# Kernel optimization log

Measured on AMD Instinct MI355X. Metric: run time of the kernel, lower is better.

## Reference

```python
import jax, jax.numpy as jnp
import numpy as np

N = 20000
E = 640000
F_IN = 128
HID = 64
HEADS = 4
OUT = 10
NUM_GRAPHS = 128
NEG_SLOPE = 0.2
BN_EPS = 1e-5


def setup_inputs() -> dict:
    key = jax.random.key(0)
    ks = jax.random.split(key, 24)
    x = jax.random.normal(ks[0], (N, F_IN), dtype=jnp.float32)
    edge_index = jax.random.randint(ks[1], (2, E), 0, N, dtype=jnp.int32)
    batch = jnp.sort(jax.random.randint(ks[2], (N,), 0, NUM_GRAPHS, dtype=jnp.int32))
    s = 0.05
    HC = HEADS * HID  # 256
    inp = {
        'x': x, 'edge_index': edge_index, 'batch': batch,
        # GATConv 1: in=128 -> heads*64, concat
        'W1': jax.random.normal(ks[3], (F_IN, HC)) * s,
        'as1': jax.random.normal(ks[4], (HEADS, HID)) * s,
        'ad1': jax.random.normal(ks[5], (HEADS, HID)) * s,
        'b1': jnp.zeros((HC,), jnp.float32),
        'g1': jnp.ones((HC,), jnp.float32),
        'be1': jnp.zeros((HC,), jnp.float32),
        # GATConv 2: in=256 -> heads*64, concat
        'W2': jax.random.normal(ks[6], (HC, HC)) * s,
        'as2': jax.random.normal(ks[7], (HEADS, HID)) * s,
        'ad2': jax.random.normal(ks[8], (HEADS, HID)) * s,
        'b2': jnp.zeros((HC,), jnp.float32),
        'g2': jnp.ones((HC,), jnp.float32),
        'be2': jnp.zeros((HC,), jnp.float32),
        # GATConv 3: in=256 -> 64, concat=False (mean over heads)
        'W3': jax.random.normal(ks[9], (HC, HC)) * s,
        'as3': jax.random.normal(ks[10], (HEADS, HID)) * s,
        'ad3': jax.random.normal(ks[11], (HEADS, HID)) * s,
        'b3': jnp.zeros((HID,), jnp.float32),
        # final Linear 64 -> 10
        'Wlin': jax.random.normal(ks[12], (HID, OUT)) * s,
        'blin': jnp.zeros((OUT,), jnp.float32),
    }
    return inp


def _gat_conv(x, src, dst, W, a_src, a_dst, b, concat):
    # PyG GATConv: h = x @ W -> [N,H,C]; alpha_e = leaky_relu(as[src]+ad[dst]);
    # softmax over edges grouped by destination; scatter-add alpha*h[src].
    h = (x @ W).reshape(N, HEADS, HID)
    a_s = jnp.einsum('nhc,hc->nh', h, a_src)  # [N,H]
    a_d = jnp.einsum('nhc,hc->nh', h, a_dst)
    e = jax.nn.leaky_relu(a_s[src] + a_d[dst], NEG_SLOPE)  # [E,H]
    m = jax.ops.segment_max(e, dst, num_segments=N)  # per-dst max, stable softmax
    e = jnp.exp(e - m[dst])
    denom = jax.ops.segment_sum(e, dst, num_segments=N)
    alpha = e / (denom[dst] + 1e-16)  # [E,H]
    out = jax.ops.segment_sum(h[src] * alpha[:, :, None], dst, num_segments=N)  # [N,H,C]
    if concat:
        out = out.reshape(N, HEADS * HID)
    else:
        out = out.mean(axis=1)
    return out + b


def _bn(x, g, b):
    # BatchNorm1d (training-mode batch statistics)
    mu = x.mean(0)
    var = x.var(0)
    return (x - mu) * jax.lax.rsqrt(var + BN_EPS) * g + b


def reference(x, edge_index, batch, W1, as1, ad1, b1, g1, be1,
              W2, as2, ad2, b2, g2, be2, W3, as3, ad3, b3, Wlin, blin):
    # add self-loops (PyG GATConv default add_self_loops=True)
    loops = jnp.arange(N, dtype=edge_index.dtype)
    src = jnp.concatenate([edge_index[0], loops])
    dst = jnp.concatenate([edge_index[1], loops])

    xs = []
    h = _gat_conv(x, src, dst, W1, as1, ad1, b1, concat=True)
    h = _bn(h, g1, be1)
    xs.append(h)
    h = jax.nn.elu(h)  # dropout is identity in eval mode

    h = _gat_conv(h, src, dst, W2, as2, ad2, b2, concat=True)
    h = _bn(h, g2, be2)
    xs.append(h)
    h = jax.nn.elu(h)

    h = _gat_conv(h, src, dst, W3, as3, ad3, b3, concat=False)
    xs.append(h)

    # global_mean_pool over graphs
    sums = jax.ops.segment_sum(h, batch, num_segments=NUM_GRAPHS)
    cnt = jax.ops.segment_sum(jnp.ones((N,), h.dtype), batch, num_segments=NUM_GRAPHS)
    pooled = sums / jnp.maximum(cnt, 1.0)[:, None]
    xs.append(pooled)

    out = pooled @ Wlin + blin
    return (out, *xs)
```

## Files before the change

### kernel.cpp

```cpp
#include <hip/hip_runtime.h>
#include <hip/hip_bf16.h>
#include <math.h>

#define N_NODES 20000
#define N_EDGES 640000
#define F_IN 128
#define HID 64
#define HEADS 4
#define HC 256
#define OUT_DIM 10
#define NUM_GRAPHS 128
#define NEG_SLOPE 0.2f
#define BN_EPS 1e-5f

typedef short bf16s;
using bf16x8 = __attribute__((ext_vector_type(8))) short;
using bf16x4 = __attribute__((ext_vector_type(4))) short;
using f32x4 = __attribute__((ext_vector_type(4))) float;

__device__ __forceinline__ float bs2f(short s) {
    unsigned int u = ((unsigned int)(unsigned short)s) << 16;
    return __builtin_bit_cast(float, u);
}
__device__ __forceinline__ short f2bs(float f) {
    unsigned int u = __builtin_bit_cast(unsigned int, f);
    unsigned int r = u + 0x7FFFu + ((u >> 16) & 1u);
    return (short)(r >> 16);
}


__global__ void fill_i32(int* p, int n, int val) {
    int tid = blockIdx.x * blockDim.x + threadIdx.x;
    if (tid < n) p[tid] = val;
}

__global__ void fill_f32(float* p, int n, float val) {
    int tid = blockIdx.x * blockDim.x + threadIdx.x;
    if (tid < n) p[tid] = val;
}

__global__ void conv_bf16(const float* __restrict__ in, bf16s* __restrict__ out, int n4) {
    int tid = blockIdx.x * blockDim.x + threadIdx.x;
    if (tid >= n4) return;
    float4 v = reinterpret_cast<const float4*>(in)[tid];
    bf16x4 o;
    o[0] = f2bs(v.x); o[1] = f2bs(v.y); o[2] = f2bs(v.z); o[3] = f2bs(v.w);
    reinterpret_cast<bf16x4*>(out)[tid] = o;
}

__global__ void prep_weights(const float* __restrict__ W1, const float* __restrict__ W2,
                             const float* __restrict__ W3,
                             bf16s* __restrict__ Wt1, bf16s* __restrict__ Wt2,
                             bf16s* __restrict__ Wt3) {
    int tid = blockIdx.x * blockDim.x + threadIdx.x;
    if (tid < HC * F_IN) {
        int c = tid >> 7, k = tid & (F_IN - 1);
        Wt1[tid] = f2bs(W1[(size_t)k * HC + c]);
    } else if (tid < HC * F_IN + HC * HC) {
        int t = tid - HC * F_IN;
        int c = t >> 8, k = t & (HC - 1);
        Wt2[t] = f2bs(W2[(size_t)k * HC + c]);
    } else if (tid < HC * F_IN + 2 * HC * HC) {
        int t = tid - HC * F_IN - HC * HC;
        int c = t >> 8, k = t & (HC - 1);
        Wt3[t] = f2bs(W3[(size_t)k * HC + c]);
    }
}


__global__ void count_deg(const int* __restrict__ ei_dst, int* deg, int E) {
    int tid = blockIdx.x * blockDim.x + threadIdx.x;
    if (tid < E) atomicAdd(&deg[ei_dst[tid]], 1);
}

__global__ void scan_deg(const int* __restrict__ deg, int* __restrict__ rowptr,
                         int* __restrict__ cursor, int n) {
    __shared__ int wsum[16];
    __shared__ int carry_s;
    int tid = threadIdx.x;
    int wid = tid >> 6, lane = tid & 63;
    if (tid == 0) { carry_s = 0; rowptr[0] = 0; }
    __syncthreads();
    for (int base = 0; base < n; base += 1024) {
        int i = base + tid;
        int v = (i < n) ? deg[i] : 0;
        int x = v;
        #pragma unroll
        for (int off = 1; off < 64; off <<= 1) {
            int t = __shfl_up(x, off);
            if (lane >= off) x += t;
        }
        if (lane == 63) wsum[wid] = x;
        __syncthreads();
        if (tid == 0) {
            int acc = carry_s;
            #pragma unroll
            for (int w = 0; w < 16; w++) { int t = wsum[w]; wsum[w] = acc; acc += t; }
            carry_s = acc;
        }
        __syncthreads();
        int inc = x + wsum[wid];
        if (i < n) { rowptr[i + 1] = inc; cursor[i] = inc - v; }
        __syncthreads();
    }
}

__global__ void fill_csr(const int* __restrict__ ei, int* cursor, int* esrc, int E, int n) {
    int tid = blockIdx.x * blockDim.x + threadIdx.x;
    if (tid < E) {
        int src = ei[tid];
        int dst = ei[E + tid];
        int pos = atomicAdd(&cursor[dst], 1);
        esrc[pos] = src;
    } else if (tid < E + n) {
        int node = tid - E;
        int pos = atomicAdd(&cursor[node], 1);
        esrc[pos] = node;
    }
}


__global__ __launch_bounds__(256) void gemm_bf16(
        const bf16s* __restrict__ A, const bf16s* __restrict__ Wt,
        bf16s* __restrict__ Hout,
        const float* __restrict__ a_src, const float* __restrict__ a_dst,
        float* __restrict__ asb, float* __restrict__ adb,
        int M, int K) {
    __shared__ bf16s As[128][72];
    __shared__ bf16s Bs[64][72];
    int tid = threadIdx.x;
    int wave = tid >> 6, lane = tid & 63;
    int row0 = blockIdx.x * 128;
    int head = blockIdx.y;
    int col0 = head * 64;
    int lr = lane & 15, lk = lane >> 4;

    f32x4 acc[2][4];
    #pragma unroll
    for (int i = 0; i < 2; i++)
        #pragma unroll
        for (int j = 0; j < 4; j++)
            acc[i][j] = (f32x4){0.f, 0.f, 0.f, 0.f};

    for (int k0 = 0; k0 < K; k0 += 64) {
        #pragma unroll
        for (int i = 0; i < 4; i++) {
            int idx = tid + i * 256;
            int r = idx >> 3, ch = idx & 7;
            int gr = row0 + r;
            bf16x8 v = {};
            if (gr < M) v = *reinterpret_cast<const bf16x8*>(A + (size_t)gr * K + k0 + ch * 8);
            *reinterpret_cast<bf16x8*>(&As[r][ch * 8]) = v;
        }
        #pragma unroll
        for (int i = 0; i < 2; i++) {
            int idx = tid + i * 256;
            int r = idx >> 3, ch = idx & 7;
            bf16x8 v = *reinterpret_cast<const bf16x8*>(Wt + (size_t)(col0 + r) * K + k0 + ch * 8);
            *reinterpret_cast<bf16x8*>(&Bs[r][ch * 8]) = v;
        }
        __syncthreads();
        #pragma unroll
        for (int ks = 0; ks < 2; ks++) {
            bf16x8 bfr[4];
            #pragma unroll
            for (int j = 0; j < 4; j++)
                bfr[j] = *reinterpret_cast<const bf16x8*>(&Bs[j * 16 + lr][ks * 32 + lk * 8]);
            #pragma unroll
            for (int i = 0; i < 2; i++) {
                bf16x8 afr = *reinterpret_cast<const bf16x8*>(&As[wave * 32 + i * 16 + lr][ks * 32 + lk * 8]);
                #pragma unroll
                for (int j = 0; j < 4; j++)
                    acc[i][j] = __builtin_amdgcn_mfma_f32_16x16x32_bf16(afr, bfr[j], acc[i][j], 0, 0, 0);
            }
        }
        __syncthreads();
    }

    #pragma unroll
    for (int i = 0; i < 2; i++) {
        #pragma unroll
        for (int q = 0; q < 4; q++) {
            int r = row0 + wave * 32 + i * 16 + lk * 4 + q;
            if (r < M) {
                #pragma unroll
                for (int j = 0; j < 4; j++) {
                    int c = col0 + j * 16 + lr;
                    Hout[(size_t)r * HC + c] = f2bs(acc[i][j][q]);
                }
            }
        }
    }

    float asv0 = a_src[col0 + 0 * 16 + lr], asv1 = a_src[col0 + 1 * 16 + lr];
    float asv2 = a_src[col0 + 2 * 16 + lr], asv3 = a_src[col0 + 3 * 16 + lr];
    float adv0 = a_dst[col0 + 0 * 16 + lr], adv1 = a_dst[col0 + 1 * 16 + lr];
    float adv2 = a_dst[col0 + 2 * 16 + lr], adv3 = a_dst[col0 + 3 * 16 + lr];
    #pragma unroll
    for (int i = 0; i < 2; i++) {
        #pragma unroll
        for (int q = 0; q < 4; q++) {
            float ps = acc[i][0][q] * asv0 + acc[i][1][q] * asv1 + acc[i][2][q] * asv2 + acc[i][3][q] * asv3;
            float pd = acc[i][0][q] * adv0 + acc[i][1][q] * adv1 + acc[i][2][q] * adv2 + acc[i][3][q] * adv3;
            #pragma unroll
            for (int off = 1; off < 16; off <<= 1) {
                ps += __shfl_xor(ps, off);
                pd += __shfl_xor(pd, off);
            }
            int r = row0 + wave * 32 + i * 16 + lk * 4 + q;
            if (lr == 0 && r < M) {
                asb[r * HEADS + head] = ps;
                adb[r * HEADS + head] = pd;
            }
        }
    }
}


__device__ __forceinline__ float lrelu(float x) { return x > 0.f ? x : NEG_SLOPE * x; }

template<int MODE>
__global__ __launch_bounds__(256) void gat_aggregate(
        const bf16s* __restrict__ hfeat,
        const float* __restrict__ asb, const float* __restrict__ adb,
        const int* __restrict__ rowptr, const int* __restrict__ esrc,
        const float* __restrict__ bias,
        float* __restrict__ out) {
    __shared__ float4 exps[4][128];
    __shared__ int    srcs[4][128];
    int wid = threadIdx.x >> 6, lane = threadIdx.x & 63;
    int d = blockIdx.x * 4 + wid;
    int start = rowptr[d], end = rowptr[d + 1];
    int deg = end - start;

    float adv0 = adb[d * HEADS + 0], adv1 = adb[d * HEADS + 1];
    float adv2 = adb[d * HEADS + 2], adv3 = adb[d * HEADS + 3];

    float s0 = 0.f, s1 = 0.f, s2 = 0.f, s3 = 0.f;
    for (int j = start + lane; j < end; j += 64) {
        int s = esrc[j];
        const float4 av = *reinterpret_cast<const float4*>(asb + (size_t)s * HEADS);
        float e0 = __expf(lrelu(av.x + adv0));
        float e1 = __expf(lrelu(av.y + adv1));
        float e2 = __expf(lrelu(av.z + adv2));
        float e3 = __expf(lrelu(av.w + adv3));
        int idx = j - start;
        if (idx < 128) {
            float4 ev; ev.x = e0; ev.y = e1; ev.z = e2; ev.w = e3;
            exps[wid][idx] = ev;
            srcs[wid][idx] = s;
        }
        s0 += e0; s1 += e1; s2 += e2; s3 += e3;
    }
    #pragma unroll
    for (int off = 32; off > 0; off >>= 1) {
        s0 += __shfl_xor(s0, off);
        s1 += __shfl_xor(s1, off);
        s2 += __shfl_xor(s2, off);
        s3 += __shfl_xor(s3, off);
    }
    float r0 = 1.f / (s0 + 1e-16f), r1 = 1.f / (s1 + 1e-16f);
    float r2 = 1.f / (s2 + 1e-16f), r3 = 1.f / (s3 + 1e-16f);

    int half = lane >> 5;
    int cl = lane & 31;
    int hsel = cl >> 3;
    float rdh = (hsel == 0) ? r0 : (hsel == 1) ? r1 : (hsel == 2) ? r2 : r3;
    float adh = (hsel == 0) ? adv0 : (hsel == 1) ? adv1 : (hsel == 2) ? adv2 : adv3;

    float a0 = 0.f, a1 = 0.f, a2 = 0.f, a3 = 0.f, a4 = 0.f, a5 = 0.f, a6 = 0.f, a7 = 0.f;
    float b0 = 0.f, b1 = 0.f, b2 = 0.f, b3 = 0.f, b4 = 0.f, b5 = 0.f, b6 = 0.f, b7 = 0.f;

    int nfull = deg & ~3;
    for (int j = 0; j < nfull; j += 4) {
        int iA = j + half;
        int iB = j + 2 + half;
        int sA, sB;
        float alA, alB;
        if (iB < 128) {
            sA = srcs[wid][iA];
            sB = srcs[wid][iB];
            alA = reinterpret_cast<const float*>(&exps[wid][iA])[hsel] * rdh;
            alB = reinterpret_cast<const float*>(&exps[wid][iB])[hsel] * rdh;
        } else {
            sA = (iA < 128) ? srcs[wid][iA] : esrc[start + iA];
            sB = esrc[start + iB];
            alA = (iA < 128) ? reinterpret_cast<const float*>(&exps[wid][iA])[hsel] * rdh
                             : __expf(lrelu(asb[(size_t)sA * HEADS + hsel] + adh)) * rdh;
            alB = __expf(lrelu(asb[(size_t)sB * HEADS + hsel] + adh)) * rdh;
        }
        const bf16x8 vA = *reinterpret_cast<const bf16x8*>(hfeat + (size_t)sA * HC + cl * 8);
        const bf16x8 vB = *reinterpret_cast<const bf16x8*>(hfeat + (size_t)sB * HC + cl * 8);
        a0 += alA * bs2f(vA[0]); a1 += alA * bs2f(vA[1]);
        a2 += alA * bs2f(vA[2]); a3 += alA * bs2f(vA[3]);
        a4 += alA * bs2f(vA[4]); a5 += alA * bs2f(vA[5]);
        a6 += alA * bs2f(vA[6]); a7 += alA * bs2f(vA[7]);
        b0 += alB * bs2f(vB[0]); b1 += alB * bs2f(vB[1]);
        b2 += alB * bs2f(vB[2]); b3 += alB * bs2f(vB[3]);
        b4 += alB * bs2f(vB[4]); b5 += alB * bs2f(vB[5]);
        b6 += alB * bs2f(vB[6]); b7 += alB * bs2f(vB[7]);
    }
    for (int j = nfull + half; j < deg; j += 2) {
        int s = (j < 128) ? srcs[wid][j] : esrc[start + j];
        float al = (j < 128) ? reinterpret_cast<const float*>(&exps[wid][j])[hsel] * rdh
                             : __expf(lrelu(asb[(size_t)s * HEADS + hsel] + adh)) * rdh;
        const bf16x8 v = *reinterpret_cast<const bf16x8*>(hfeat + (size_t)s * HC + cl * 8);
        a0 += al * bs2f(v[0]); a1 += al * bs2f(v[1]);
        a2 += al * bs2f(v[2]); a3 += al * bs2f(v[3]);
        a4 += al * bs2f(v[4]); a5 += al * bs2f(v[5]);
        a6 += al * bs2f(v[6]); a7 += al * bs2f(v[7]);
    }
    float av0 = a0 + b0, av1 = a1 + b1, av2 = a2 + b2, av3 = a3 + b3;
    float av4 = a4 + b4, av5 = a5 + b5, av6 = a6 + b6, av7 = a7 + b7;

    av0 += __shfl_xor(av0, 32); av1 += __shfl_xor(av1, 32);
    av2 += __shfl_xor(av2, 32); av3 += __shfl_xor(av3, 32);
    av4 += __shfl_xor(av4, 32); av5 += __shfl_xor(av5, 32);
    av6 += __shfl_xor(av6, 32); av7 += __shfl_xor(av7, 32);

    if constexpr (MODE == 0) {
        if (half == 0) {
            const float4 bb0 = *reinterpret_cast<const float4*>(bias + cl * 8);
            const float4 bb1 = *reinterpret_cast<const float4*>(bias + cl * 8 + 4);
            av0 += bb0.x; av1 += bb0.y; av2 += bb0.z; av3 += bb0.w;
            av4 += bb1.x; av5 += bb1.y; av6 += bb1.z; av7 += bb1.w;
            float4 o0; o0.x = av0; o0.y = av1; o0.z = av2; o0.w = av3;
            float4 o1; o1.x = av4; o1.y = av5; o1.z = av6; o1.w = av7;
            *reinterpret_cast<float4*>(out + (size_t)d * HC + cl * 8) = o0;
            *reinterpret_cast<float4*>(out + (size_t)d * HC + cl * 8 + 4) = o1;
        }
    } else {
        float h0 = av0 + __shfl_xor(av0, 8); h0 += __shfl_xor(h0, 16);
        float h1 = av1 + __shfl_xor(av1, 8); h1 += __shfl_xor(h1, 16);
        float h2 = av2 + __shfl_xor(av2, 8); h2 += __shfl_xor(h2, 16);
        float h3 = av3 + __shfl_xor(av3, 8); h3 += __shfl_xor(h3, 16);
        float h4 = av4 + __shfl_xor(av4, 8); h4 += __shfl_xor(h4, 16);
        float h5 = av5 + __shfl_xor(av5, 8); h5 += __shfl_xor(h5, 16);
        float h6 = av6 + __shfl_xor(av6, 8); h6 += __shfl_xor(h6, 16);
        float h7 = av7 + __shfl_xor(av7, 8); h7 += __shfl_xor(h7, 16);
        if (half == 0 && cl < 8) {
            int c = cl * 8;
            float4 o0, o1;
            o0.x = 0.25f * h0 + bias[c + 0]; o0.y = 0.25f * h1 + bias[c + 1];
            o0.z = 0.25f * h2 + bias[c + 2]; o0.w = 0.25f * h3 + bias[c + 3];
            o1.x = 0.25f * h4 + bias[c + 4]; o1.y = 0.25f * h5 + bias[c + 5];
            o1.z = 0.25f * h6 + bias[c + 6]; o1.w = 0.25f * h7 + bias[c + 7];
            *reinterpret_cast<float4*>(out + (size_t)d * HID + c) = o0;
            *reinterpret_cast<float4*>(out + (size_t)d * HID + c + 4) = o1;
        }
    }
}


__global__ void bn_stats(const float* __restrict__ x, float* colsum, float* colsq, int n) {
    int col = threadIdx.x;
    float s = 0.f, q = 0.f;
    for (int r = blockIdx.x; r < n; r += gridDim.x) {
        float v = x[(size_t)r * HC + col];
        s += v;
        q += v * v;
    }
    atomicAdd(&colsum[col], s);
    atomicAdd(&colsq[col], q);
}

__global__ void bn_finalize(float* colsum, float* colsq,
                            const float* __restrict__ g, const float* __restrict__ be,
                            float* scale, float* shift, int n) {
    int col = threadIdx.x;
    float mu = colsum[col] / (float)n;
    float var = colsq[col] / (float)n - mu * mu;
    float sc = g[col] * rsqrtf(var + BN_EPS);
    scale[col] = sc;
    shift[col] = be[col] - mu * sc;
    colsum[col] = 0.f;
    colsq[col] = 0.f;
}

__global__ void bn_apply_elu(const float* __restrict__ x,
                             const float* __restrict__ scale, const float* __restrict__ shift,
                             float* __restrict__ xs_out, bf16s* __restrict__ act, int n) {
    int col = threadIdx.x;
    float sc = scale[col], sh = shift[col];
    for (int r = blockIdx.x; r < n; r += gridDim.x) {
        float v = x[(size_t)r * HC + col];
        float y = v * sc + sh;
        xs_out[(size_t)r * HC + col] = y;
        float e = y > 0.f ? y : __expf(y) - 1.f;
        act[(size_t)r * HC + col] = f2bs(e);
    }
}


__global__ __launch_bounds__(256) void pool_final(
        const float* __restrict__ xs2, const int* __restrict__ batch,
        const float* __restrict__ Wlin, const float* __restrict__ blin,
        float* __restrict__ pooled_out, float* __restrict__ out_final) {
    __shared__ float red[4][HID];
    int g = blockIdx.x;
    int tid = threadIdx.x;
    int w = tid >> 6, lane = tid & 63;

    int lo = 0, hi = N_NODES;
    while (lo < hi) { int mid = (lo + hi) >> 1; if (batch[mid] < g) lo = mid + 1; else hi = mid; }
    int a = lo;
    lo = 0; hi = N_NODES;
    while (lo < hi) { int mid = (lo + hi) >> 1; if (batch[mid] < g + 1) lo = mid + 1; else hi = mid; }
    int b = lo;

    float acc = 0.f;
    for (int n = a + w; n < b; n += 4) acc += xs2[(size_t)n * HID + lane];
    red[w][lane] = acc;
    __syncthreads();

    if (w == 0) {
        float pooled = (red[0][lane] + red[1][lane] + red[2][lane] + red[3][lane])
                       / fmaxf((float)(b - a), 1.f);
        pooled_out[g * HID + lane] = pooled;
        #pragma unroll
        for (int o = 0; o < OUT_DIM; o++) {
            float p = pooled * Wlin[lane * OUT_DIM + o];
            #pragma unroll
            for (int off = 32; off > 0; off >>= 1) p += __shfl_xor(p, off);
            if (lane == 0) out_final[g * OUT_DIM + o] = p + blin[o];
        }
    }
}


extern "C" void kernel_launch(void* const* d_in, const int* in_sizes, int n_in,
                              void* d_out, int out_size, void* d_ws, size_t ws_size,
                              hipStream_t stream) {
    const float* x     = (const float*)d_in[0];
    const int*   ei    = (const int*)d_in[1];
    const int*   batch = (const int*)d_in[2];
    const float* W1  = (const float*)d_in[3];
    const float* as1 = (const float*)d_in[4];
    const float* ad1 = (const float*)d_in[5];
    const float* b1  = (const float*)d_in[6];
    const float* g1  = (const float*)d_in[7];
    const float* be1 = (const float*)d_in[8];
    const float* W2  = (const float*)d_in[9];
    const float* as2 = (const float*)d_in[10];
    const float* ad2 = (const float*)d_in[11];
    const float* b2  = (const float*)d_in[12];
    const float* g2  = (const float*)d_in[13];
    const float* be2 = (const float*)d_in[14];
    const float* W3  = (const float*)d_in[15];
    const float* as3 = (const float*)d_in[16];
    const float* ad3 = (const float*)d_in[17];
    const float* b3  = (const float*)d_in[18];
    const float* Wlin = (const float*)d_in[19];
    const float* blin = (const float*)d_in[20];

    float* out_final = (float*)d_out;
    float* xs0 = out_final + NUM_GRAPHS * OUT_DIM;
    float* xs1 = xs0 + (size_t)N_NODES * HC;
    float* xs2 = xs1 + (size_t)N_NODES * HC;
    float* pooled_out = xs2 + (size_t)N_NODES * HID;

    char* p = (char*)d_ws;
    auto alloc = [&](size_t bytes) { char* r = p; p += (bytes + 255) & ~(size_t)255; return (void*)r; };
    bf16s* hfeat  = (bf16s*)alloc((size_t)N_NODES * HC * 2);
    bf16s* actC   = (bf16s*)alloc((size_t)N_NODES * HC * 2);
    bf16s* xb     = (bf16s*)alloc((size_t)N_NODES * F_IN * 2);
    float* gatB   = (float*)alloc((size_t)N_NODES * HC * 4);
    bf16s* Wt1    = (bf16s*)alloc((size_t)HC * F_IN * 2);
    bf16s* Wt2    = (bf16s*)alloc((size_t)HC * HC * 2);
    bf16s* Wt3    = (bf16s*)alloc((size_t)HC * HC * 2);
    float* asb    = (float*)alloc((size_t)N_NODES * HEADS * 4);
    float* adb    = (float*)alloc((size_t)N_NODES * HEADS * 4);
    int*   deg    = (int*)alloc((size_t)N_NODES * 4);
    int*   cursor = (int*)alloc((size_t)N_NODES * 4);
    int*   rowptr = (int*)alloc((size_t)(N_NODES + 1) * 4);
    int*   esrc   = (int*)alloc((size_t)(N_EDGES + N_NODES) * 4);
    float* colstats = (float*)alloc(2 * HC * 4);
    float* colsum = colstats;
    float* colsq  = colstats + HC;
    float* scale  = (float*)alloc(HC * 4);
    float* shift  = (float*)alloc(HC * 4);

    const int ETOT = N_EDGES + N_NODES;

    fill_i32<<<(N_NODES + 255) / 256, 256, 0, stream>>>(deg, N_NODES, 1);
    count_deg<<<(N_EDGES + 255) / 256, 256, 0, stream>>>(ei + N_EDGES, deg, N_EDGES);
    scan_deg<<<1, 1024, 0, stream>>>(deg, rowptr, cursor, N_NODES);
    fill_csr<<<(ETOT + 255) / 256, 256, 0, stream>>>(ei, cursor, esrc, N_EDGES, N_NODES);

    conv_bf16<<<((N_NODES * F_IN / 4) + 255) / 256, 256, 0, stream>>>(x, xb, N_NODES * F_IN / 4);
    prep_weights<<<(HC * F_IN + 2 * HC * HC + 255) / 256, 256, 0, stream>>>(W1, W2, W3, Wt1, Wt2, Wt3);
    fill_f32<<<2, 256, 0, stream>>>(colstats, 2 * HC, 0.f);

    int agg_blocks = N_NODES / 4;
    dim3 ggrid((N_NODES + 127) / 128, HEADS);

    {
        gemm_bf16<<<ggrid, 256, 0, stream>>>(xb, Wt1, hfeat, as1, ad1, asb, adb, N_NODES, F_IN);
        gat_aggregate<0><<<agg_blocks, 256, 0, stream>>>(hfeat, asb, adb, rowptr, esrc, b1, gatB);
        bn_stats<<<512, 256, 0, stream>>>(gatB, colsum, colsq, N_NODES);
        bn_finalize<<<1, 256, 0, stream>>>(colsum, colsq, g1, be1, scale, shift, N_NODES);
        bn_apply_elu<<<2048, 256, 0, stream>>>(gatB, scale, shift, xs0, actC, N_NODES);
    }
    {
        gemm_bf16<<<ggrid, 256, 0, stream>>>(actC, Wt2, hfeat, as2, ad2, asb, adb, N_NODES, HC);
        gat_aggregate<0><<<agg_blocks, 256, 0, stream>>>(hfeat, asb, adb, rowptr, esrc, b2, gatB);
        bn_stats<<<512, 256, 0, stream>>>(gatB, colsum, colsq, N_NODES);
        bn_finalize<<<1, 256, 0, stream>>>(colsum, colsq, g2, be2, scale, shift, N_NODES);
        bn_apply_elu<<<2048, 256, 0, stream>>>(gatB, scale, shift, xs1, actC, N_NODES);
    }
    {
        gemm_bf16<<<ggrid, 256, 0, stream>>>(actC, Wt3, hfeat, as3, ad3, asb, adb, N_NODES, HC);
        gat_aggregate<1><<<agg_blocks, 256, 0, stream>>>(hfeat, asb, adb, rowptr, esrc, b3, xs2);
    }
    pool_final<<<NUM_GRAPHS, 256, 0, stream>>>(xs2, batch, Wlin, blin, pooled_out, out_final);
}
```

Measured before the change: 350.9 us.

## Merge prep kernels, fuse BN finalize via last-block counter, unroll aggregation by 8

Folds the fill, bf16 conversion and weight transpose kernels into one prep kernel, and folds the self-loop +1 into the scan. BN finalize now runs inside the stats kernel, where the last block to arrive on an atomic counter computes the result. The aggregation gather loop is unrolled to four independent edges per half-wave with extra accumulators, to raise memory-level parallelism. The changes cut kernel launches, at the cost of higher register pressure in the aggregate and a more complex tail loop.

After: 364.2 us. +3.8%, slower.

```diff
diff --git a/kernel.cpp b/kernel.cpp
--- a/kernel.cpp
+++ b/kernel.cpp
@@ -12,6 +12,7 @@
 #define NUM_GRAPHS 128
 #define NEG_SLOPE 0.2f
 #define BN_EPS 1e-5f
+#define CONV_N (N_NODES * F_IN / 4)
 
 typedef short bf16s;
 using bf16x8 = __attribute__((ext_vector_type(8))) short;
@@ -29,42 +30,33 @@
 }
 
 
-__global__ void fill_i32(int* p, int n, int val) {
+__global__ void prep_all(const float* __restrict__ x, bf16s* __restrict__ xb,
+                         const float* __restrict__ W1, const float* __restrict__ W2,
+                         const float* __restrict__ W3,
+                         bf16s* __restrict__ Wt1, bf16s* __restrict__ Wt2,
+                         bf16s* __restrict__ Wt3,
+                         int* __restrict__ deg, float* __restrict__ colstats,
+                         int* __restrict__ counter) {
     int tid = blockIdx.x * blockDim.x + threadIdx.x;
-    if (tid < n) p[tid] = val;
-}
-
-__global__ void fill_f32(float* p, int n, float val) {
-    int tid = blockIdx.x * blockDim.x + threadIdx.x;
-    if (tid < n) p[tid] = val;
-}
-
-__global__ void conv_bf16(const float* __restrict__ in, bf16s* __restrict__ out, int n4) {
-    int tid = blockIdx.x * blockDim.x + threadIdx.x;
-    if (tid >= n4) return;
-    float4 v = reinterpret_cast<const float4*>(in)[tid];
-    bf16x4 o;
-    o[0] = f2bs(v.x); o[1] = f2bs(v.y); o[2] = f2bs(v.z); o[3] = f2bs(v.w);
-    reinterpret_cast<bf16x4*>(out)[tid] = o;
-}
-
-__global__ void prep_weights(const float* __restrict__ W1, const float* __restrict__ W2,
-                             const float* __restrict__ W3,
-                             bf16s* __restrict__ Wt1, bf16s* __restrict__ Wt2,
-                             bf16s* __restrict__ Wt3) {
-    int tid = blockIdx.x * blockDim.x + threadIdx.x;
-    if (tid < HC * F_IN) {
-        int c = tid >> 7, k = tid & (F_IN - 1);
-        Wt1[tid] = f2bs(W1[(size_t)k * HC + c]);
-    } else if (tid < HC * F_IN + HC * HC) {
-        int t = tid - HC * F_IN;
-        int c = t >> 8, k = t & (HC - 1);
-        Wt2[t] = f2bs(W2[(size_t)k * HC + c]);
-    } else if (tid < HC * F_IN + 2 * HC * HC) {
-        int t = tid - HC * F_IN - HC * HC;
-        int c = t >> 8, k = t & (HC - 1);
-        Wt3[t] = f2bs(W3[(size_t)k * HC + c]);
-    }
+    if (tid < CONV_N) {
+        float4 v = reinterpret_cast<const float4*>(x)[tid];
+        bf16x4 o;
+        o[0] = f2bs(v.x); o[1] = f2bs(v.y); o[2] = f2bs(v.z); o[3] = f2bs(v.w);
+        reinterpret_cast<bf16x4*>(xb)[tid] = o;
+        return;
+    }
+    tid -= CONV_N;
+    if (tid < HC * F_IN) { int c = tid >> 7, k = tid & 127; Wt1[tid] = f2bs(W1[(size_t)k * HC + c]); return; }
+    tid -= HC * F_IN;
+    if (tid < HC * HC) { int c = tid >> 8, k = tid & 255; Wt2[tid] = f2bs(W2[(size_t)k * HC + c]); return; }
+    tid -= HC * HC;
+    if (tid < HC * HC) { int c = tid >> 8, k = tid & 255; Wt3[tid] = f2bs(W3[(size_t)k * HC + c]); return; }
+    tid -= HC * HC;
+    if (tid < N_NODES) { deg[tid] = 0; return; }
+    tid -= N_NODES;
+    if (tid < 2 * HC) { colstats[tid] = 0.f; return; }
+    tid -= 2 * HC;
+    if (tid == 0) *counter = 0;
 }
 
 
@@ -83,7 +75,7 @@
     __syncthreads();
     for (int base = 0; base < n; base += 1024) {
         int i = base + tid;
-        int v = (i < n) ? deg[i] : 0;
+        int v = (i < n) ? (deg[i] + 1) : 0;
         int x = v;
         #pragma unroll
         for (int off = 1; off < 64; off <<= 1) {
@@ -267,30 +259,41 @@
     int hsel = cl >> 3;
     float rdh = (hsel == 0) ? r0 : (hsel == 1) ? r1 : (hsel == 2) ? r2 : r3;
     float adh = (hsel == 0) ? adv0 : (hsel == 1) ? adv1 : (hsel == 2) ? adv2 : adv3;
+    const float* expf_base = reinterpret_cast<const float*>(&exps[wid][0]);
 
     float a0 = 0.f, a1 = 0.f, a2 = 0.f, a3 = 0.f, a4 = 0.f, a5 = 0.f, a6 = 0.f, a7 = 0.f;
     float b0 = 0.f, b1 = 0.f, b2 = 0.f, b3 = 0.f, b4 = 0.f, b5 = 0.f, b6 = 0.f, b7 = 0.f;
-
-    int nfull = deg & ~3;
-    for (int j = 0; j < nfull; j += 4) {
-        int iA = j + half;
-        int iB = j + 2 + half;
-        int sA, sB;
-        float alA, alB;
-        if (iB < 128) {
-            sA = srcs[wid][iA];
-            sB = srcs[wid][iB];
-            alA = reinterpret_cast<const float*>(&exps[wid][iA])[hsel] * rdh;
-            alB = reinterpret_cast<const float*>(&exps[wid][iB])[hsel] * rdh;
+    float c0 = 0.f, c1 = 0.f, c2 = 0.f, c3 = 0.f, c4 = 0.f, c5 = 0.f, c6 = 0.f, c7 = 0.f;
+    float d0 = 0.f, d1 = 0.f, d2 = 0.f, d3 = 0.f, d4 = 0.f, d5 = 0.f, d6 = 0.f, d7 = 0.f;
+
+    int nfull8 = deg & ~7;
+    for (int j = 0; j < nfull8; j += 8) {
+        int i0 = j + half, i1 = j + 2 + half, i2 = j + 4 + half, i3 = j + 6 + half;
+        int sA, sB, sC, sD;
+        float alA, alB, alC, alD;
+        if (i3 < 128) {
+            sA = srcs[wid][i0]; sB = srcs[wid][i1]; sC = srcs[wid][i2]; sD = srcs[wid][i3];
+            alA = expf_base[i0 * 4 + hsel] * rdh;
+            alB = expf_base[i1 * 4 + hsel] * rdh;
+            alC = expf_base[i2 * 4 + hsel] * rdh;
+            alD = expf_base[i3 * 4 + hsel] * rdh;
         } else {
-            sA = (iA < 128) ? srcs[wid][iA] : esrc[start + iA];
-            sB = esrc[start + iB];
-            alA = (iA < 128) ? reinterpret_cast<const float*>(&exps[wid][iA])[hsel] * rdh
+            sA = (i0 < 128) ? srcs[wid][i0] : esrc[start + i0];
+            sB = (i1 < 128) ? srcs[wid][i1] : esrc[start + i1];
+            sC = (i2 < 128) ? srcs[wid][i2] : esrc[start + i2];
+            sD = esrc[start + i3];
+            alA = (i0 < 128) ? expf_base[i0 * 4 + hsel] * rdh
                              : __expf(lrelu(asb[(size_t)sA * HEADS + hsel] + adh)) * rdh;
-            alB = __expf(lrelu(asb[(size_t)sB * HEADS + hsel] + adh)) * rdh;
+            alB = (i1 < 128) ? expf_base[i1 * 4 + hsel] * rdh
+                             : __expf(lrelu(asb[(size_t)sB * HEADS + hsel] + adh)) * rdh;
+            alC = (i2 < 128) ? expf_base[i2 * 4 + hsel] * rdh
+                             : __expf(lrelu(asb[(size_t)sC * HEADS + hsel] + adh)) * rdh;
+            alD = __expf(lrelu(asb[(size_t)sD * HEADS + hsel] + adh)) * rdh;
         }
         const bf16x8 vA = *reinterpret_cast<const bf16x8*>(hfeat + (size_t)sA * HC + cl * 8);
         const bf16x8 vB = *reinterpret_cast<const bf16x8*>(hfeat + (size_t)sB * HC + cl * 8);
+        const bf16x8 vC = *reinterpret_cast<const bf16x8*>(hfeat + (size_t)sC * HC + cl * 8);
+        const bf16x8 vD = *reinterpret_cast<const bf16x8*>(hfeat + (size_t)sD * HC + cl * 8);
         a0 += alA * bs2f(vA[0]); a1 += alA * bs2f(vA[1]);
         a2 += alA * bs2f(vA[2]); a3 += alA * bs2f(vA[3]);
         a4 += alA * bs2f(vA[4]); a5 += alA * bs2f(vA[5]);
@@ -299,10 +302,18 @@
         b2 += alB * bs2f(vB[2]); b3 += alB * bs2f(vB[3]);
         b4 += alB * bs2f(vB[4]); b5 += alB * bs2f(vB[5]);
         b6 += alB * bs2f(vB[6]); b7 += alB * bs2f(vB[7]);
-    }
-    for (int j = nfull + half; j < deg; j += 2) {
+        c0 += alC * bs2f(vC[0]); c1 += alC * bs2f(vC[1]);
+        c2 += alC * bs2f(vC[2]); c3 += alC * bs2f(vC[3]);
+        c4 += alC * bs2f(vC[4]); c5 += alC * bs2f(vC[5]);
+        c6 += alC * bs2f(vC[6]); c7 += alC * bs2f(vC[7]);
+        d0 += alD * bs2f(vD[0]); d1 += alD * bs2f(vD[1]);
+        d2 += alD * bs2f(vD[2]); d3 += alD * bs2f(vD[3]);
+        d4 += alD * bs2f(vD[4]); d5 += alD * bs2f(vD[5]);
+        d6 += alD * bs2f(vD[6]); d7 += alD * bs2f(vD[7]);
+    }
+    for (int j = nfull8 + half; j < deg; j += 2) {
         int s = (j < 128) ? srcs[wid][j] : esrc[start + j];
-        float al = (j < 128) ? reinterpret_cast<const float*>(&exps[wid][j])[hsel] * rdh
+        float al = (j < 128) ? expf_base[j * 4 + hsel] * rdh
                              : __expf(lrelu(asb[(size_t)s * HEADS + hsel] + adh)) * rdh;
         const bf16x8 v = *reinterpret_cast<const bf16x8*>(hfeat + (size_t)s * HC + cl * 8);
         a0 += al * bs2f(v[0]); a1 += al * bs2f(v[1]);
@@ -310,8 +321,10 @@
         a4 += al * bs2f(v[4]); a5 += al * bs2f(v[5]);
         a6 += al * bs2f(v[6]); a7 += al * bs2f(v[7]);
     }
-    float av0 = a0 + b0, av1 = a1 + b1, av2 = a2 + b2, av3 = a3 + b3;
-    float av4 = a4 + b4, av5 = a5 + b5, av6 = a6 + b6, av7 = a7 + b7;
+    float av0 = (a0 + b0) + (c0 + d0), av1 = (a1 + b1) + (c1 + d1);
+    float av2 = (a2 + b2) + (c2 + d2), av3 = (a3 + b3) + (c3 + d3);
+    float av4 = (a4 + b4) + (c4 + d4), av5 = (a5 + b5) + (c5 + d5);
+    float av6 = (a6 + b6) + (c6 + d6), av7 = (a7 + b7) + (c7 + d7);
 
     av0 += __shfl_xor(av0, 32); av1 += __shfl_xor(av1, 32);
     av2 += __shfl_xor(av2, 32); av3 += __shfl_xor(av3, 32);
@@ -352,7 +365,10 @@
 }
 
 
-__global__ void bn_stats(const float* __restrict__ x, float* colsum, float* colsq, int n) {
+__global__ void bn_stats_fin(const float* __restrict__ x, float* colsum, float* colsq,
+                             const float* __restrict__ g, const float* __restrict__ be,
+                             float* scale, float* shift, int* counter, int n) {
+    __shared__ int lastFlag;
     int col = threadIdx.x;
     float s = 0.f, q = 0.f;
     for (int r = blockIdx.x; r < n; r += gridDim.x) {
@@ -362,19 +378,26 @@
     }
     atomicAdd(&colsum[col], s);
     atomicAdd(&colsq[col], q);
-}
-
-__global__ void bn_finalize(float* colsum, float* colsq,
-                            const float* __restrict__ g, const float* __restrict__ be,
-                            float* scale, float* shift, int n) {
-    int col = threadIdx.x;
-    float mu = colsum[col] / (float)n;
-    float var = colsq[col] / (float)n - mu * mu;
-    float sc = g[col] * rsqrtf(var + BN_EPS);
-    scale[col] = sc;
-    shift[col] = be[col] - mu * sc;
-    colsum[col] = 0.f;
-    colsq[col] = 0.f;
+    __syncthreads();
+    if (threadIdx.x == 0) {
+        __threadfence();
+        int prev = atomicAdd(counter, 1);
+        lastFlag = (prev == (int)gridDim.x - 1) ? 1 : 0;
+    }
+    __syncthreads();
+    if (lastFlag) {
+        __threadfence();
+        float cs = ((volatile float*)colsum)[col];
+        float cq = ((volatile float*)colsq)[col];
+        float mu = cs / (float)n;
+        float var = cq / (float)n - mu * mu;
+        float sc = g[col] * rsqrtf(var + BN_EPS);
+        scale[col] = sc;
+        shift[col] = be[col] - mu * sc;
+        colsum[col] = 0.f;
+        colsq[col] = 0.f;
+        if (threadIdx.x == 0) *counter = 0;
+    }
 }
 
 __global__ void bn_apply_elu(const float* __restrict__ x,
@@ -479,33 +502,30 @@
     float* colsq  = colstats + HC;
     float* scale  = (float*)alloc(HC * 4);
     float* shift  = (float*)alloc(HC * 4);
+    int*   counter = (int*)alloc(256);
 
     const int ETOT = N_EDGES + N_NODES;
-
-    fill_i32<<<(N_NODES + 255) / 256, 256, 0, stream>>>(deg, N_NODES, 1);
+    const int PREP_TOT = CONV_N + HC * F_IN + 2 * HC * HC + N_NODES + 2 * HC + 1;
+
+    prep_all<<<(PREP_TOT + 255) / 256, 256, 0, stream>>>(x, xb, W1, W2, W3, Wt1, Wt2, Wt3,
+                                                         deg, colstats, counter);
     count_deg<<<(N_EDGES + 255) / 256, 256, 0, stream>>>(ei + N_EDGES, deg, N_EDGES);
     scan_deg<<<1, 1024, 0, stream>>>(deg, rowptr, cursor, N_NODES);
     fill_csr<<<(ETOT + 255) / 256, 256, 0, stream>>>(ei, cursor, esrc, N_EDGES, N_NODES);
 
-    conv_bf16<<<((N_NODES * F_IN / 4) + 255) / 256, 256, 0, stream>>>(x, xb, N_NODES * F_IN / 4);
-    prep_weights<<<(HC * F_IN + 2 * HC * HC + 255) / 256, 256, 0, stream>>>(W1, W2, W3, Wt1, Wt2, Wt3);
-    fill_f32<<<2, 256, 0, stream>>>(colstats, 2 * HC, 0.f);
-
     int agg_blocks = N_NODES / 4;
     dim3 ggrid((N_NODES + 127) / 128, HEADS);
 
     {
         gemm_bf16<<<ggrid, 256, 0, stream>>>(xb, Wt1, hfeat, as1, ad1, asb, adb, N_NODES, F_IN);
         gat_aggregate<0><<<agg_blocks, 256, 0, stream>>>(hfeat, asb, adb, rowptr, esrc, b1, gatB);
-        bn_stats<<<512, 256, 0, stream>>>(gatB, colsum, colsq, N_NODES);
-        bn_finalize<<<1, 256, 0, stream>>>(colsum, colsq, g1, be1, scale, shift, N_NODES);
+        bn_stats_fin<<<512, 256, 0, stream>>>(gatB, colsum, colsq, g1, be1, scale, shift, counter, N_NODES);
         bn_apply_elu<<<2048, 256, 0, stream>>>(gatB, scale, shift, xs0, actC, N_NODES);
     }
     {
         gemm_bf16<<<ggrid, 256, 0, stream>>>(actC, Wt2, hfeat, as2, ad2, asb, adb, N_NODES, HC);
         gat_aggregate<0><<<agg_blocks, 256, 0, stream>>>(hfeat, asb, adb, rowptr, esrc, b2, gatB);
-        bn_stats<<<512, 256, 0, stream>>>(gatB, colsum, colsq, N_NODES);
-        bn_finalize<<<1, 256, 0, stream>>>(colsum, colsq, g2, be2, scale, shift, N_NODES);
+        bn_stats_fin<<<512, 256, 0, stream>>>(gatB, colsum, colsq, g2, be2, scale, shift, counter, N_NODES);
         bn_apply_elu<<<2048, 256, 0, stream>>>(gatB, scale, shift, xs1, actC, N_NODES);
     }
     {
```
